# Performance work log

Hardware: AMD Instinct MI355X
Metric: run time of the kernel (lower is better)

The kernel has to match this reference:

```python
import jax, jax.numpy as jnp
import numpy as np

B, S, F, DV, H, DH, L = 32, 600, 9, 1024, 16, 64, 2


def setup_inputs() -> dict:
    key = jax.random.key(0)
    ks = jax.random.split(key, 24)
    w = lambda k, shape, s=0.05: jax.random.normal(k, shape, dtype=jnp.float32) * s
    return {
        "x": w(ks[0], (B, S, F), 1.0),
        "enc_in_W": w(ks[1], (F, DV)), "enc_in_b": w(ks[2], (DV,)),
        "Wq": w(ks[3], (L, H, DV, DH)), "bq": w(ks[4], (L, H, DH)),
        "Wk": w(ks[5], (L, H, DV, DH)), "bk": w(ks[6], (L, H, DH)),
        "Wv": w(ks[7], (L, H, DV, DH)), "bv": w(ks[8], (L, H, DH)),
        "Wo": w(ks[9], (L, DV, DV)), "bo": w(ks[10], (L, DV)),
        "W1": w(ks[11], (L, DV, DV)), "b1": w(ks[12], (L, DV)),
        "W2": w(ks[13], (L, DV, DV)), "b2": w(ks[14], (L, DV)),
        "ln1_w": jnp.ones((L, DV)), "ln1_b": jnp.zeros((L, DV)),
        "ln2_w": jnp.ones((L, DV)), "ln2_b": jnp.zeros((L, DV)),
        "out_W": w(ks[15], (DV, F)), "out_b": w(ks[16], (F,)),
    }


def _layernorm(v, g, b):
    mu = v.mean(-1, keepdims=True)
    var = v.var(-1, keepdims=True)  # biased, matches torch LayerNorm
    return (v - mu) / jnp.sqrt(var + 1e-5) * g + b


def reference(x, enc_in_W, enc_in_b, Wq, bq, Wk, bk, Wv, bv, Wo, bo,
              W1, b1, W2, b2, ln1_w, ln1_b, ln2_w, ln2_b, out_W, out_b):
    # enc_input_fc; pe skipped (code checks pe_mode == 'stardard', never true)
    h = x @ enc_in_W + enc_in_b  # [B,S,DV]
    scale = 1.0 / jnp.sqrt(jnp.float32(DH))
    for l in range(L):
        q = jnp.einsum('bsd,hdk->bhsk', h, Wq[l]) + bq[l][None, :, None, :]
        k = jnp.einsum('bsd,hdk->bhsk', h, Wk[l]) + bk[l][None, :, None, :]
        v = jnp.einsum('bsd,hdk->bhsk', h, Wv[l]) + bv[l][None, :, None, :]
        attn = jax.nn.softmax(jnp.einsum('bhsk,bhtk->bhst', q, k) * scale, axis=-1)
        ctx = jnp.einsum('bhst,bhtk->bhsk', attn, v)  # [B,H,S,DH]
        # torch: stack(heads, dim=-1) -> [B,S,DH,H], then flatten(start_dim=2)
        a = ctx.transpose(0, 2, 3, 1).reshape(B, S, DH * H)
        attn_out = a @ Wo[l] + bo[l]
        x1 = _layernorm(h + attn_out, ln1_w[l], ln1_b[l])
        ff = jax.nn.elu(x1 @ W2[l] + b2[l]) @ W1[l] + b1[l]  # fc1(elu(fc2(x1)))
        h = _layernorm(x1 + ff, ln2_w[l], ln2_b[l])
    out = h @ out_W + out_b  # [B,S,F]; in_seq_len == out_seq_len -> no out_seq_fc
    return out
```

## Files before the change

kernel.cpp:

```cpp
#include <hip/hip_runtime.h>

typedef unsigned short u16;
typedef unsigned int u32;
typedef __attribute__((ext_vector_type(8))) short shortx8;
typedef __attribute__((ext_vector_type(4))) float floatx4;
typedef __attribute__((ext_vector_type(4))) u32 uintx4;
typedef __attribute__((ext_vector_type(2))) u32 uintx2;

#define AS1 __attribute__((address_space(1)))
#define AS3 __attribute__((address_space(3)))

__device__ __forceinline__ float bf2f(u16 u) {
  return __builtin_bit_cast(float, ((u32)u) << 16);
}
__device__ __forceinline__ u16 f2bf(float f) {
  u32 i = __builtin_bit_cast(u32, f);
  u32 r = (i + 0x7fffu + ((i >> 16) & 1u)) >> 16;
  return (u16)r;
}

__launch_bounds__(256)
__global__ void pack_qkv_t(const float* __restrict__ W, u16* __restrict__ dst) {
  __shared__ u16 T[64][72];
  const int kt = blockIdx.x, y = blockIdx.y;
  const int l = y >> 4, h = y & 15;
  const int t = threadIdx.x;
  const int rr = t >> 2, cq = (t & 3) * 16;
  const float* src = W + ((size_t)y * 1024 + kt * 64 + rr) * 64 + cq;
#pragma unroll
  for (int e4 = 0; e4 < 4; ++e4) {
    float4 f = *(const float4*)(src + e4 * 4);
    T[cq + e4 * 4 + 0][rr] = f2bf(f.x);
    T[cq + e4 * 4 + 1][rr] = f2bf(f.y);
    T[cq + e4 * 4 + 2][rr] = f2bf(f.z);
    T[cq + e4 * 4 + 3][rr] = f2bf(f.w);
  }
  __syncthreads();
  const int dd = t >> 2, kq = (t & 3) * 16;
  u16* drow = dst + (size_t)l * 3145728 + ((size_t)h * 64 + dd) * 1024 + kt * 64 + kq;
  *(uintx4*)(drow) = *(const uintx4*)&T[dd][kq];
  *(uintx4*)(drow + 8) = *(const uintx4*)&T[dd][kq + 8];
}

__launch_bounds__(256)
__global__ void pack_sq_t(const float* __restrict__ W, u16* __restrict__ dst) {
  __shared__ u16 T[64][72];
  const int ct = blockIdx.x & 15, rt = blockIdx.x >> 4, l = blockIdx.y;
  const int t = threadIdx.x;
  const int rr = t >> 2, cq = (t & 3) * 16;
  const float* src = W + (size_t)l * 1048576 + (size_t)(rt * 64 + rr) * 1024 + ct * 64 + cq;
#pragma unroll
  for (int e4 = 0; e4 < 4; ++e4) {
    float4 f = *(const float4*)(src + e4 * 4);
    T[cq + e4 * 4 + 0][rr] = f2bf(f.x);
    T[cq + e4 * 4 + 1][rr] = f2bf(f.y);
    T[cq + e4 * 4 + 2][rr] = f2bf(f.z);
    T[cq + e4 * 4 + 3][rr] = f2bf(f.w);
  }
  __syncthreads();
  const int cc = t >> 2, rq = (t & 3) * 16;
  u16* drow = dst + (size_t)l * 1048576 + (size_t)(ct * 64 + cc) * 1024 + rt * 64 + rq;
  *(uintx4*)(drow) = *(const uintx4*)&T[cc][rq];
  *(uintx4*)(drow + 8) = *(const uintx4*)&T[cc][rq + 8];
}

__launch_bounds__(256)
__global__ void pack_bias(const float* __restrict__ bq, const float* __restrict__ bk,
                          const float* __restrict__ bv, float* __restrict__ bias) {
  const int i = blockIdx.x * 256 + threadIdx.x;
  const int l = i / 3072, n = i % 3072;
  const int which = n >> 10, nn = n & 1023;
  const float* s = (which == 0) ? bq : (which == 1) ? bk : bv;
  bias[i] = s[l * 1024 + nn];
}

__launch_bounds__(256)
__global__ void enc_kernel(const float* __restrict__ x, const float* __restrict__ W,
                           const float* __restrict__ bias, u16* __restrict__ h) {
  const size_t i = (size_t)blockIdx.x * 256 + threadIdx.x;
  const int m = (int)(i >> 10), n = (int)(i & 1023);
  const float* xr = x + (size_t)m * 9;
  float acc = bias[n];
#pragma unroll
  for (int f = 0; f < 9; ++f) acc += xr[f] * W[f * 1024 + n];
  h[i] = f2bf(acc);
}

template <int EPI>
__launch_bounds__(256)
__global__ void gemm_bt(const u16* __restrict__ A, int lda,
                        const u16* __restrict__ Bt,
                        const float* __restrict__ bias,
                        const u16* __restrict__ R, int ldr,
                        u16* __restrict__ C, int ldc) {
  constexpr int K = 1024;
  __shared__ u16 sh[128 * 136];
  u16* As = sh;
  u16* Bs = sh + 8192;
  const int tid = threadIdx.x;
  const int lane = tid & 63;
  const int w = tid >> 6;
  const int wr = w >> 1, wc = w & 1;
  const int m0 = blockIdx.y * 128, n0 = blockIdx.x * 128;

  floatx4 acc[4][4];
#pragma unroll
  for (int i = 0; i < 4; ++i)
#pragma unroll
    for (int j = 0; j < 4; ++j) acc[i][j] = (floatx4){0.f, 0.f, 0.f, 0.f};

  const u16* Ab = A + (size_t)m0 * lda;
  const u16* Bb = Bt + (size_t)n0 * K;

  for (int k0 = 0; k0 < K; k0 += 64) {
#pragma unroll
    for (int p = 0; p < 4; ++p) {
      const int o = p * 4096 + tid * 16;
      const int row = o >> 7;
      const int ke = (o & 127) >> 1;
      __builtin_amdgcn_global_load_lds((const AS1 void*)(Ab + (size_t)row * lda + (k0 + ke)),
                                       (AS3 void*)((char*)As + o), 16, 0, 0);
      __builtin_amdgcn_global_load_lds((const AS1 void*)(Bb + (size_t)row * K + (k0 + ke)),
                                       (AS3 void*)((char*)Bs + o), 16, 0, 0);
    }
    __syncthreads();
#pragma unroll
    for (int ks = 0; ks < 2; ++ks) {
      shortx8 af[4], bfr[4];
#pragma unroll
      for (int i = 0; i < 4; ++i) {
        const int ar = wr * 64 + i * 16 + (lane & 15);
        af[i] = *(const shortx8*)&As[ar * 64 + ks * 32 + (lane >> 4) * 8];
        const int br = wc * 64 + i * 16 + (lane & 15);
        bfr[i] = *(const shortx8*)&Bs[br * 64 + ks * 32 + (lane >> 4) * 8];
      }
#pragma unroll
      for (int i = 0; i < 4; ++i)
#pragma unroll
        for (int j = 0; j < 4; ++j)
          acc[i][j] = __builtin_amdgcn_mfma_f32_16x16x32_bf16(af[i], bfr[j], acc[i][j], 0, 0, 0);
    }
    __syncthreads();
  }

  const int lr = (lane >> 4) * 4, lc = lane & 15;
#pragma unroll
  for (int i = 0; i < 4; ++i) {
#pragma unroll
    for (int j = 0; j < 4; ++j) {
      const int col = wc * 64 + j * 16 + lc;
      const float bv = bias[n0 + col];
#pragma unroll
      for (int r = 0; r < 4; ++r) {
        const int row = wr * 64 + i * 16 + lr + r;
        float v = acc[i][j][r] + bv;
        if (EPI == 2) v = v > 0.f ? v : expm1f(v);
        sh[row * 136 + col] = f2bf(v);
      }
    }
  }
  __syncthreads();

  {
    const int row = tid >> 1, seg = (tid & 1) * 64;
    u16* crow = C + (size_t)(m0 + row) * ldc + n0 + seg;
    const u16* srow = sh + row * 136 + seg;
    if (EPI == 1) {
      const u16* rrow = R + (size_t)(m0 + row) * ldr + n0 + seg;
#pragma unroll
      for (int q = 0; q < 8; ++q) {
        uintx4 cv = *(const uintx4*)(srow + q * 8);
        uintx4 rv = *(const uintx4*)(rrow + q * 8);
        uintx4 ov;
#pragma unroll
        for (int e = 0; e < 4; ++e) {
          const u32 c2 = cv[e], r2 = rv[e];
          const float lo = bf2f((u16)(c2 & 0xffffu)) + bf2f((u16)(r2 & 0xffffu));
          const float hi = bf2f((u16)(c2 >> 16)) + bf2f((u16)(r2 >> 16));
          ov[e] = (u32)f2bf(lo) | ((u32)f2bf(hi) << 16);
        }
        *(uintx4*)(crow + q * 8) = ov;
      }
    } else {
#pragma unroll
      for (int q = 0; q < 8; ++q)
        *(uintx4*)(crow + q * 8) = *(const uintx4*)(srow + q * 8);
    }
  }
}

__launch_bounds__(256)
__global__ void attn_mfma(const u16* __restrict__ qkv, u16* __restrict__ aout) {
  const int qt = blockIdx.x, bh = blockIdx.y;
  const int b = bh >> 4, h = bh & 15;
  const int tid = threadIdx.x, lane = tid & 63, w = tid >> 6;
  const int g = lane >> 4, lq = lane & 15;

  __shared__ u16 K_ld[128 * 72];
  __shared__ u16 Vt[64 * 136];
  __shared__ u16 P_ld[4][16 * 136];

  const size_t bbase = (size_t)b * 600 * 3072;
  const int q0 = qt * 64 + w * 16;

  shortx8 aq[2];
  {
    const int s = q0 + lq;
    if (s < 600) {
      const u16* qp = qkv + bbase + (size_t)s * 3072 + h * 64 + g * 8;
      aq[0] = *(const shortx8*)qp;
      aq[1] = *(const shortx8*)(qp + 32);
    } else {
      aq[0] = (shortx8){0, 0, 0, 0, 0, 0, 0, 0};
      aq[1] = (shortx8){0, 0, 0, 0, 0, 0, 0, 0};
    }
  }

  floatx4 Oa[4];
#pragma unroll
  for (int db = 0; db < 4; ++db) Oa[db] = (floatx4){0.f, 0.f, 0.f, 0.f};
  float m[4], l[4];
#pragma unroll
  for (int r = 0; r < 4; ++r) { m[r] = -1e30f; l[r] = 0.f; }

  for (int ch = 0; ch < 5; ++ch) {
    const int t0 = ch * 128;
    __syncthreads();
    {
      const int tloc = tid >> 1, dhalf = (tid & 1) * 32;
      const int tg = t0 + tloc;
      if (tg < 600) {
        const u16* kp = qkv + bbase + (size_t)tg * 3072 + 1024 + h * 64 + dhalf;
        const u16* vp = kp + 1024;
#pragma unroll
        for (int c = 0; c < 4; ++c)
          *(uintx4*)&K_ld[tloc * 72 + dhalf + c * 8] = *(const uintx4*)(kp + c * 8);
#pragma unroll
        for (int c = 0; c < 4; ++c) {
          shortx8 vv = *(const shortx8*)(vp + c * 8);
#pragma unroll
          for (int e = 0; e < 8; ++e)
            Vt[(dhalf + c * 8 + e) * 136 + tloc] = (u16)vv[e];
        }
      } else {
        const uintx4 z4 = (uintx4){0, 0, 0, 0};
#pragma unroll
        for (int c = 0; c < 4; ++c)
          *(uintx4*)&K_ld[tloc * 72 + dhalf + c * 8] = z4;
#pragma unroll
        for (int c = 0; c < 4; ++c)
#pragma unroll
          for (int e = 0; e < 8; ++e)
            Vt[(dhalf + c * 8 + e) * 136 + tloc] = 0;
      }
    }
    __syncthreads();

    floatx4 S[8];
#pragma unroll
    for (int jb = 0; jb < 8; ++jb) {
      S[jb] = (floatx4){0.f, 0.f, 0.f, 0.f};
#pragma unroll
      for (int ks = 0; ks < 2; ++ks) {
        shortx8 bk = *(const shortx8*)&K_ld[(jb * 16 + lq) * 72 + ks * 32 + g * 8];
        S[jb] = __builtin_amdgcn_mfma_f32_16x16x32_bf16(aq[ks], bk, S[jb], 0, 0, 0);
      }
    }
#pragma unroll
    for (int jb = 0; jb < 8; ++jb) {
      const int tg = t0 + jb * 16 + lq;
      const bool ok = tg < 600;
#pragma unroll
      for (int r = 0; r < 4; ++r) S[jb][r] = ok ? S[jb][r] * 0.125f : -1e30f;
    }

    float scale[4];
#pragma unroll
    for (int r = 0; r < 4; ++r) {
      float v = S[0][r];
#pragma unroll
      for (int jb = 1; jb < 8; ++jb) v = fmaxf(v, S[jb][r]);
      v = fmaxf(v, __shfl_xor(v, 1));
      v = fmaxf(v, __shfl_xor(v, 2));
      v = fmaxf(v, __shfl_xor(v, 4));
      v = fmaxf(v, __shfl_xor(v, 8));
      const float mn = fmaxf(m[r], v);
      scale[r] = __expf(m[r] - mn);
      m[r] = mn;
      l[r] *= scale[r];
    }
#pragma unroll
    for (int db = 0; db < 4; ++db)
#pragma unroll
      for (int r = 0; r < 4; ++r) Oa[db][r] *= scale[r];

    float sums[4] = {0.f, 0.f, 0.f, 0.f};
#pragma unroll
    for (int jb = 0; jb < 8; ++jb)
#pragma unroll
      for (int r = 0; r < 4; ++r) {
        const float p = __expf(S[jb][r] - m[r]);
        sums[r] += p;
        P_ld[w][(g * 4 + r) * 136 + jb * 16 + lq] = f2bf(p);
      }
#pragma unroll
    for (int r = 0; r < 4; ++r) {
      float v = sums[r];
      v += __shfl_xor(v, 1);
      v += __shfl_xor(v, 2);
      v += __shfl_xor(v, 4);
      v += __shfl_xor(v, 8);
      l[r] += v;
    }

#pragma unroll
    for (int ks = 0; ks < 4; ++ks) {
      shortx8 ap = *(const shortx8*)&P_ld[w][lq * 136 + ks * 32 + g * 8];
#pragma unroll
      for (int db = 0; db < 4; ++db) {
        shortx8 bv = *(const shortx8*)&Vt[(db * 16 + lq) * 136 + ks * 32 + g * 8];
        Oa[db] = __builtin_amdgcn_mfma_f32_16x16x32_bf16(ap, bv, Oa[db], 0, 0, 0);
      }
    }
  }

#pragma unroll
  for (int r = 0; r < 4; ++r) {
    const int sg = q0 + g * 4 + r;
    if (sg < 600) {
      const float inv = 1.f / l[r];
      u16* orow = aout + ((size_t)(b * 600 + sg)) * 1024 + h;
#pragma unroll
      for (int db = 0; db < 4; ++db)
        orow[(size_t)(db * 16 + lq) * 16] = f2bf(Oa[db][r] * inv);
    }
  }
}

__launch_bounds__(256)
__global__ void ln_kernel(const u16* __restrict__ y, int ldy,
                          const float* __restrict__ g, const float* __restrict__ be,
                          u16* __restrict__ o, int ldo) {
  const int row = blockIdx.x, tid = threadIdx.x;
  const int lane = tid & 63, wv = tid >> 6;
  const u16* yr = y + (size_t)row * ldy;
  const int c = tid * 4;
  const uintx2 yv = *(const uintx2*)&yr[c];
  float v0 = bf2f((u16)(yv[0] & 0xffffu)), v1 = bf2f((u16)(yv[0] >> 16));
  float v2 = bf2f((u16)(yv[1] & 0xffffu)), v3 = bf2f((u16)(yv[1] >> 16));
  float s = v0 + v1 + v2 + v3;
  float q = v0 * v0 + v1 * v1 + v2 * v2 + v3 * v3;
#pragma unroll
  for (int m = 32; m; m >>= 1) {
    s += __shfl_xor(s, m);
    q += __shfl_xor(q, m);
  }
  __shared__ float red[2][4];
  if (lane == 0) {
    red[0][wv] = s;
    red[1][wv] = q;
  }
  __syncthreads();
  s = red[0][0] + red[0][1] + red[0][2] + red[0][3];
  q = red[1][0] + red[1][1] + red[1][2] + red[1][3];
  const float mu = s * (1.f / 1024.f);
  const float var = q * (1.f / 1024.f) - mu * mu;
  const float rstd = rsqrtf(var + 1e-5f);
  const float4 gv = *(const float4*)&g[c];
  const float4 bev = *(const float4*)&be[c];
  const float o0 = (v0 - mu) * rstd * gv.x + bev.x;
  const float o1 = (v1 - mu) * rstd * gv.y + bev.y;
  const float o2 = (v2 - mu) * rstd * gv.z + bev.z;
  const float o3 = (v3 - mu) * rstd * gv.w + bev.w;
  uintx2 ov;
  ov[0] = (u32)f2bf(o0) | ((u32)f2bf(o1) << 16);
  ov[1] = (u32)f2bf(o2) | ((u32)f2bf(o3) << 16);
  *(uintx2*)&o[(size_t)row * ldo + c] = ov;
}

__launch_bounds__(256)
__global__ void out_kernel(const u16* __restrict__ h, const float* __restrict__ W,
                           const float* __restrict__ bias, float* __restrict__ out) {
  const int m = blockIdx.x * 4 + (threadIdx.x >> 6);
  const int lane = threadIdx.x & 63;
  float acc[9];
#pragma unroll
  for (int f = 0; f < 9; ++f) acc[f] = 0.f;
  const u16* hr = h + (size_t)m * 1024;
#pragma unroll 4
  for (int j = 0; j < 16; ++j) {
    const int k = lane + j * 64;
    const float hv = bf2f(hr[k]);
    const float* wr = W + (size_t)k * 9;
#pragma unroll
    for (int f = 0; f < 9; ++f) acc[f] += hv * wr[f];
  }
#pragma unroll
  for (int f = 0; f < 9; ++f)
#pragma unroll
    for (int mm = 32; mm; mm >>= 1) acc[f] += __shfl_xor(acc[f], mm);
  if (lane < 9) out[(size_t)m * 9 + lane] = acc[lane] + bias[lane];
}

extern "C" void kernel_launch(void* const* d_in, const int* in_sizes, int n_in,
                              void* d_out, int out_size, void* d_ws, size_t ws_size,
                              hipStream_t stream) {
  (void)in_sizes; (void)n_in; (void)out_size; (void)ws_size;
  const float* x     = (const float*)d_in[0];
  const float* encW  = (const float*)d_in[1];
  const float* encB  = (const float*)d_in[2];
  const float* Wq    = (const float*)d_in[3];
  const float* bq    = (const float*)d_in[4];
  const float* Wk    = (const float*)d_in[5];
  const float* bk    = (const float*)d_in[6];
  const float* Wv    = (const float*)d_in[7];
  const float* bv    = (const float*)d_in[8];
  const float* Wo    = (const float*)d_in[9];
  const float* bo    = (const float*)d_in[10];
  const float* W1    = (const float*)d_in[11];
  const float* b1    = (const float*)d_in[12];
  const float* W2    = (const float*)d_in[13];
  const float* b2    = (const float*)d_in[14];
  const float* ln1w  = (const float*)d_in[15];
  const float* ln1b  = (const float*)d_in[16];
  const float* ln2w  = (const float*)d_in[17];
  const float* ln2b  = (const float*)d_in[18];
  const float* outW  = (const float*)d_in[19];
  const float* outB  = (const float*)d_in[20];
  float* out = (float*)d_out;

  char* ws = (char*)d_ws;
  size_t off = 0;
  auto alloc = [&](size_t bytes) -> void* {
    void* p = ws + off;
    off += (bytes + 255) & ~(size_t)255;
    return p;
  };
  u16* h    = (u16*)alloc(19660800ull * 2);
  u16* qkv  = (u16*)alloc(58982400ull * 2);
  u16* abuf = (u16*)alloc(19660800ull * 2);
  u16* Bqkv = (u16*)alloc(6291456ull * 2);
  u16* Bwo  = (u16*)alloc(2097152ull * 2);
  u16* Bw1  = (u16*)alloc(2097152ull * 2);
  u16* Bw2  = (u16*)alloc(2097152ull * 2);
  float* bqkv = (float*)alloc(6144ull * 4);
  u16* ybuf = qkv;
  u16* x1   = qkv + 1024;
  u16* mid  = qkv + 2048;
  u16* y2   = abuf;

  pack_qkv_t<<<dim3(16, 32), 256, 0, stream>>>(Wq, Bqkv);
  pack_qkv_t<<<dim3(16, 32), 256, 0, stream>>>(Wk, Bqkv + 1048576);
  pack_qkv_t<<<dim3(16, 32), 256, 0, stream>>>(Wv, Bqkv + 2097152);
  pack_sq_t<<<dim3(256, 2), 256, 0, stream>>>(Wo, Bwo);
  pack_sq_t<<<dim3(256, 2), 256, 0, stream>>>(W1, Bw1);
  pack_sq_t<<<dim3(256, 2), 256, 0, stream>>>(W2, Bw2);
  pack_bias<<<24, 256, 0, stream>>>(bq, bk, bv, bqkv);
  enc_kernel<<<76800, 256, 0, stream>>>(x, encW, encB, h);

  for (int l = 0; l < 2; ++l) {
    gemm_bt<0><<<dim3(24, 150), 256, 0, stream>>>(
        h, 1024, Bqkv + (size_t)l * 3145728, bqkv + l * 3072, nullptr, 0, qkv, 3072);
    attn_mfma<<<dim3(10, 512), 256, 0, stream>>>(qkv, abuf);
    gemm_bt<1><<<dim3(8, 150), 256, 0, stream>>>(
        abuf, 1024, Bwo + (size_t)l * 1048576, bo + l * 1024, h, 1024, ybuf, 3072);
    ln_kernel<<<19200, 256, 0, stream>>>(ybuf, 3072, ln1w + l * 1024, ln1b + l * 1024, x1, 3072);
    gemm_bt<2><<<dim3(8, 150), 256, 0, stream>>>(
        x1, 3072, Bw2 + (size_t)l * 1048576, b2 + l * 1024, nullptr, 0, mid, 3072);
    gemm_bt<1><<<dim3(8, 150), 256, 0, stream>>>(
        mid, 3072, Bw1 + (size_t)l * 1048576, b1 + l * 1024, x1, 3072, y2, 1024);
    ln_kernel<<<19200, 256, 0, stream>>>(y2, 1024, ln2w + l * 1024, ln2b + l * 1024, h, 1024);
  }
  out_kernel<<<4800, 256, 0, stream>>>(h, outW, outB, out);
}
```

Baseline: 1.458 ms.

## Double-buffer GEMM LDS tiles and write epilogue directly to global

The GEMM main loop now keeps two LDS buffers for A and B and issues the global-to-LDS loads for the next K tile before computing on the current one. This overlaps memory latency with MFMA work and needs one barrier per iteration instead of two. The epilogue no longer stages through shared memory; it writes scalar bf16 values, with the residual added, straight to global memory. That uncoalesced 2-byte store pattern may cost more bandwidth than the LDS staging it replaces. LDS use doubles to 64KB, which may lower occupancy.

```diff
diff --git a/kernel.cpp b/kernel.cpp
--- a/kernel.cpp
+++ b/kernel.cpp
@@ -94,9 +94,9 @@
                         const u16* __restrict__ R, int ldr,
                         u16* __restrict__ C, int ldc) {
   constexpr int K = 1024;
-  __shared__ u16 sh[128 * 136];
-  u16* As = sh;
-  u16* Bs = sh + 8192;
+  constexpr int NT = K / 64;
+  __shared__ u16 As[2][128 * 64];
+  __shared__ u16 Bs[2][128 * 64];
   const int tid = threadIdx.x;
   const int lane = tid & 63;
   const int w = tid >> 6;
@@ -112,27 +112,35 @@
   const u16* Ab = A + (size_t)m0 * lda;
   const u16* Bb = Bt + (size_t)n0 * K;
 
-  for (int k0 = 0; k0 < K; k0 += 64) {
+  auto STAGE = [&](int buf, int k0) {
 #pragma unroll
     for (int p = 0; p < 4; ++p) {
       const int o = p * 4096 + tid * 16;
       const int row = o >> 7;
       const int ke = (o & 127) >> 1;
       __builtin_amdgcn_global_load_lds((const AS1 void*)(Ab + (size_t)row * lda + (k0 + ke)),
-                                       (AS3 void*)((char*)As + o), 16, 0, 0);
+                                       (AS3 void*)((char*)&As[buf][0] + o), 16, 0, 0);
       __builtin_amdgcn_global_load_lds((const AS1 void*)(Bb + (size_t)row * K + (k0 + ke)),
-                                       (AS3 void*)((char*)Bs + o), 16, 0, 0);
-    }
-    __syncthreads();
+                                       (AS3 void*)((char*)&Bs[buf][0] + o), 16, 0, 0);
+    }
+  };
+
+  STAGE(0, 0);
+  __syncthreads();
+  int cur = 0;
+  for (int t = 0; t < NT; ++t) {
+    if (t + 1 < NT) STAGE(cur ^ 1, (t + 1) * 64);
+    const u16* Ac = As[cur];
+    const u16* Bc = Bs[cur];
 #pragma unroll
     for (int ks = 0; ks < 2; ++ks) {
       shortx8 af[4], bfr[4];
 #pragma unroll
       for (int i = 0; i < 4; ++i) {
         const int ar = wr * 64 + i * 16 + (lane & 15);
-        af[i] = *(const shortx8*)&As[ar * 64 + ks * 32 + (lane >> 4) * 8];
+        af[i] = *(const shortx8*)&Ac[ar * 64 + ks * 32 + (lane >> 4) * 8];
         const int br = wc * 64 + i * 16 + (lane & 15);
-        bfr[i] = *(const shortx8*)&Bs[br * 64 + ks * 32 + (lane >> 4) * 8];
+        bfr[i] = *(const shortx8*)&Bc[br * 64 + ks * 32 + (lane >> 4) * 8];
       }
 #pragma unroll
       for (int i = 0; i < 4; ++i)
@@ -141,6 +149,7 @@
           acc[i][j] = __builtin_amdgcn_mfma_f32_16x16x32_bf16(af[i], bfr[j], acc[i][j], 0, 0, 0);
     }
     __syncthreads();
+    cur ^= 1;
   }
 
   const int lr = (lane >> 4) * 4, lc = lane & 15;
@@ -148,43 +157,16 @@
   for (int i = 0; i < 4; ++i) {
 #pragma unroll
     for (int j = 0; j < 4; ++j) {
-      const int col = wc * 64 + j * 16 + lc;
-      const float bv = bias[n0 + col];
+      const int col = n0 + wc * 64 + j * 16 + lc;
+      const float bv = bias[col];
 #pragma unroll
       for (int r = 0; r < 4; ++r) {
-        const int row = wr * 64 + i * 16 + lr + r;
+        const int row = m0 + wr * 64 + i * 16 + lr + r;
         float v = acc[i][j][r] + bv;
+        if (EPI == 1) v += bf2f(R[(size_t)row * ldr + col]);
         if (EPI == 2) v = v > 0.f ? v : expm1f(v);
-        sh[row * 136 + col] = f2bf(v);
-      }
-    }
-  }
-  __syncthreads();
-
-  {
-    const int row = tid >> 1, seg = (tid & 1) * 64;
-    u16* crow = C + (size_t)(m0 + row) * ldc + n0 + seg;
-    const u16* srow = sh + row * 136 + seg;
-    if (EPI == 1) {
-      const u16* rrow = R + (size_t)(m0 + row) * ldr + n0 + seg;
-#pragma unroll
-      for (int q = 0; q < 8; ++q) {
-        uintx4 cv = *(const uintx4*)(srow + q * 8);
-        uintx4 rv = *(const uintx4*)(rrow + q * 8);
-        uintx4 ov;
-#pragma unroll
-        for (int e = 0; e < 4; ++e) {
-          const u32 c2 = cv[e], r2 = rv[e];
-          const float lo = bf2f((u16)(c2 & 0xffffu)) + bf2f((u16)(r2 & 0xffffu));
-          const float hi = bf2f((u16)(c2 >> 16)) + bf2f((u16)(r2 >> 16));
-          ov[e] = (u32)f2bf(lo) | ((u32)f2bf(hi) << 16);
-        }
-        *(uintx4*)(crow + q * 8) = ov;
-      }
-    } else {
-#pragma unroll
-      for (int q = 0; q < 8; ++q)
-        *(uintx4*)(crow + q * 8) = *(const uintx4*)(srow + q * 8);
+        C[(size_t)row * ldc + col] = f2bf(v);
+      }
     }
   }
 }
```

Measured after the change: 1.569 ms. 7.6% more time.
